# Kernel tuning notes

Hardware: AMD Instinct MI355X
Metric: run time of the kernel (lower is better)

The kernel has to match this reference:

```python
import jax, jax.numpy as jnp
import numpy as np

KH = KW = 3
PAD = 1
STRIDE = 1
C_IN = 32
C_OUT = 16
H = W = 64
B = 64
H_OUT = (H - KH + 2 * PAD) // STRIDE + 1
W_OUT = (W - KW + 2 * PAD) // STRIDE + 1
S = H_OUT * W_OUT
K = C_IN * KH * KW


def unfold_2d(x):
    # x: [B, C, H, W] -> [B, C*KH*KW, S], torch.nn.functional.unfold ordering
    xp = jnp.pad(x, ((0, 0), (0, 0), (PAD, PAD), (PAD, PAD)))
    patches = []
    for i in range(KH):
        for j in range(KW):
            patches.append(xp[:, :, i:i + H_OUT * STRIDE:STRIDE, j:j + W_OUT * STRIDE:STRIDE])
    u = jnp.stack(patches, axis=2)  # [B, C, KH*KW, H_OUT, W_OUT]
    return u.reshape(x.shape[0], K, S)


def setup_inputs() -> dict:
    key = jax.random.key(0)
    k1, k2, k3 = jax.random.split(key, 3)
    X = jax.random.normal(k1, (B, C_IN, H, W), dtype=jnp.float32)
    # kaiming normal (linear): std = 1/sqrt(fan_in), fan_in = K for each location's GEMM
    weight = jax.random.normal(k2, (S, K, C_OUT), dtype=jnp.float32) / jnp.sqrt(jnp.float32(K))
    # xavier uniform over [H_OUT, W_OUT]
    lim = np.sqrt(6.0 / (H_OUT + W_OUT))
    bias = jax.random.uniform(k3, (H_OUT, W_OUT), dtype=jnp.float32, minval=-lim, maxval=lim)
    return {"X": X, "weight": weight, "bias": bias}


def reference(X, weight, bias):
    ufld = unfold_2d(X)                               # [B, K, S]
    ufld = ufld + bias.reshape(1, 1, -1)              # bias added per-location to patches
    h = jnp.einsum('bks,skc->bcs', ufld, weight)      # per-location unshared GEMM
    return h.reshape(X.shape[0], C_OUT, H_OUT, W_OUT)
```

## Files before the change

### kernel.cpp

```cpp
#include <hip/hip_runtime.h>
#include <stdint.h>
#include <stddef.h>

#define HOUT 64
#define WOUT 64
#define CIN  32
#define COUT 16
#define BATCH 64
#define SLOC 4096
#define KTOT 288
#define HPAD 66

typedef __attribute__((ext_vector_type(8))) short  short8;
typedef __attribute__((ext_vector_type(4))) float  floatx4;

static __device__ __forceinline__ unsigned short f2bf(float f) {
    union { float f; unsigned int u; } v; v.f = f;
    unsigned int u = v.u;
    unsigned int r = (u + 0x7FFFu + ((u >> 16) & 1u)) >> 16;
    return (unsigned short)r;
}

__global__ __launch_bounds__(256) void zero_border_kernel(unsigned short* __restrict__ xt) {
    int bid = blockIdx.x;
    int h1, w1;
    if (bid < 66)       { h1 = 0;  w1 = bid; }
    else if (bid < 132) { h1 = 65; w1 = bid - 66; }
    else { int r = bid - 132; h1 = (r >> 1) + 1; w1 = (r & 1) ? 65 : 0; }
    uint4* dst = (uint4*)(xt + (size_t)(h1 * HPAD + w1) * 2048);
    dst[threadIdx.x] = uint4{0u, 0u, 0u, 0u};
}

__global__ __launch_bounds__(256) void transpose_kernel(const float* __restrict__ X,
                                                        unsigned short* __restrict__ xt) {
    int h = blockIdx.x;
    int b = blockIdx.y;
    int t = threadIdx.x;
    int w  = t >> 2;
    int cg = t & 3;

    const float* xb = X + (((size_t)b * CIN + cg * 8) * HOUT + h) * WOUT + w;
    unsigned short v[8];
#pragma unroll
    for (int j = 0; j < 8; ++j)
        v[j] = f2bf(xb[(size_t)j * HOUT * WOUT]);

    uint4 pack;
    pack.x = (unsigned)v[0] | ((unsigned)v[1] << 16);
    pack.y = (unsigned)v[2] | ((unsigned)v[3] << 16);
    pack.z = (unsigned)v[4] | ((unsigned)v[5] << 16);
    pack.w = (unsigned)v[6] | ((unsigned)v[7] << 16);

    *(uint4*)(xt + (size_t)((h + 1) * HPAD + (w + 1)) * 2048 + b * CIN + cg * 8) = pack;
}

__global__ __launch_bounds__(256, 4) void varconv_kernel(const unsigned short* __restrict__ xt,
                                                         const float* __restrict__ Wg,
                                                         const float* __restrict__ bias,
                                                         float* __restrict__ out) {
    __shared__ float lds[16 * 16 * 16];

    int id = blockIdx.x;
    int lo = id & 7;
    int q4 = (id >> 3) & 3;
    int g  = ((id >> 5) << 3) | lo;
    int s0 = g * 16;
    int y  = s0 >> 6;
    int x0 = s0 & 63;
    int B0 = q4 * 16;

    int lane = threadIdx.x & 63, wv = threadIdx.x >> 6;
    int q = lane >> 4;
    int n = lane & 15;

#pragma unroll
    for (int i = 0; i < 4; ++i) {
        int sl = wv * 4 + i;
        int s  = s0 + sl;
        int x  = x0 + sl;

        const float* wb = Wg + (size_t)s * (KTOT * COUT) + (size_t)(8 * q) * 9 * COUT + n;
        float w[9][8];
#pragma unroll
        for (int t = 0; t < 9; ++t)
#pragma unroll
            for (int j = 0; j < 8; ++j)
                w[t][j] = wb[(size_t)(j * 9 + t) * COUT];

        float csum = 0.f;
        short8 bf[9];
#pragma unroll
        for (int t = 0; t < 9; ++t)
#pragma unroll
            for (int j = 0; j < 8; ++j) {
                csum += w[t][j];
                bf[t][j] = (short)f2bf(w[t][j]);
            }
        csum += __shfl_xor(csum, 16, 64);
        csum += __shfl_xor(csum, 32, 64);
        float badd = bias[s] * csum;

        const unsigned short* ab = xt + (size_t)(B0 + n) * CIN + q * 8;
        floatx4 acc = {0.f, 0.f, 0.f, 0.f};
#pragma unroll
        for (int t = 0; t < 9; ++t) {
            const int cy = t / 3, cx = t % 3;
            int pix = (y + cy) * HPAD + (x + cx);
            short8 af = *(const short8*)(ab + (size_t)pix * 2048);
            acc = __builtin_amdgcn_mfma_f32_16x16x32_bf16(af, bf[t], acc, 0, 0, 0);
        }
        int slot = q ^ (n & 3);
        floatx4 v = {acc[0] + badd, acc[1] + badd, acc[2] + badd, acc[3] + badd};
        *(floatx4*)&lds[n * 256 + sl * 16 + slot * 4] = v;
    }

    __syncthreads();

    int c   = lane >> 2;
    int slg = lane & 3;
#pragma unroll
    for (int i2 = 0; i2 < 4; ++i2) {
        int ib   = wv * 4 + i2;
        int slot = (ib >> 2) ^ (c & 3);
        float o0[4];
#pragma unroll
        for (int e = 0; e < 4; ++e)
            o0[e] = lds[c * 256 + (slg * 4 + e) * 16 + slot * 4 + (ib & 3)];
        floatx4 o = {o0[0], o0[1], o0[2], o0[3]};
        *(floatx4*)(out + ((size_t)((B0 + ib) * COUT + c)) * SLOC + s0 + slg * 4) = o;
    }
}

extern "C" void kernel_launch(void* const* d_in, const int* in_sizes, int n_in,
                              void* d_out, int out_size, void* d_ws, size_t ws_size,
                              hipStream_t stream) {
    const float* X    = (const float*)d_in[0];
    const float* Wg   = (const float*)d_in[1];
    const float* bias = (const float*)d_in[2];
    float* out = (float*)d_out;

    unsigned short* xt = (unsigned short*)d_ws;

    zero_border_kernel<<<260, 256, 0, stream>>>(xt);
    transpose_kernel<<<dim3(64, 64), 256, 0, stream>>>(X, xt);
    varconv_kernel<<<1024, 256, 0, stream>>>(xt, Wg, bias, out);
}
```

Baseline: 173.8 us.

## Precompute bf16 packed weights and bias sums in a separate prep kernel

Adds a kernel that converts the per-location fp32 weights into bf16 in MFMA operand order and precomputes the bias-times-weight-sum per location and output channel. The main conv kernel then loads coalesced 16-byte weight fragments instead of doing strided fp32 gathers and conversions. It also batches all nine activation loads ahead of the MFMA chain. The cost is an extra launch and about twice the weight memory traffic, since the packed weights are written and read again every call.

```diff
diff --git a/kernel.cpp b/kernel.cpp
--- a/kernel.cpp
+++ b/kernel.cpp
@@ -54,9 +54,49 @@
     *(uint4*)(xt + (size_t)((h + 1) * HPAD + (w + 1)) * 2048 + b * CIN + cg * 8) = pack;
 }
 
+__global__ __launch_bounds__(576) void wprep_kernel(const float* __restrict__ Wg,
+                                                    const float* __restrict__ bias,
+                                                    uint4* __restrict__ wt,
+                                                    float* __restrict__ bsum) {
+    __shared__ float red[9][16];
+    int s    = blockIdx.x;
+    int t    = threadIdx.x >> 6;
+    int lane = threadIdx.x & 63;
+    int q = lane >> 4, n = lane & 15;
+
+    const float* wb = Wg + (size_t)s * (KTOT * COUT) + (size_t)((8 * q) * 9 + t) * COUT + n;
+    float w[8];
+#pragma unroll
+    for (int j = 0; j < 8; ++j)
+        w[j] = wb[(size_t)j * 9 * COUT];
+
+    float csum = 0.f;
+    unsigned short h[8];
+#pragma unroll
+    for (int j = 0; j < 8; ++j) { csum += w[j]; h[j] = f2bf(w[j]); }
+
+    uint4 pack;
+    pack.x = (unsigned)h[0] | ((unsigned)h[1] << 16);
+    pack.y = (unsigned)h[2] | ((unsigned)h[3] << 16);
+    pack.z = (unsigned)h[4] | ((unsigned)h[5] << 16);
+    pack.w = (unsigned)h[6] | ((unsigned)h[7] << 16);
+    wt[(size_t)(s * 9 + t) * 64 + lane] = pack;
+
+    csum += __shfl_xor(csum, 16, 64);
+    csum += __shfl_xor(csum, 32, 64);
+    if (lane < 16) red[t][n] = csum;
+    __syncthreads();
+    if (threadIdx.x < 16) {
+        float tot = 0.f;
+#pragma unroll
+        for (int tt = 0; tt < 9; ++tt) tot += red[tt][threadIdx.x];
+        bsum[s * COUT + threadIdx.x] = bias[s] * tot;
+    }
+}
+
 __global__ __launch_bounds__(256, 4) void varconv_kernel(const unsigned short* __restrict__ xt,
-                                                         const float* __restrict__ Wg,
-                                                         const float* __restrict__ bias,
+                                                         const uint4* __restrict__ wt,
+                                                         const float* __restrict__ bsum,
                                                          float* __restrict__ out) {
     __shared__ float lds[16 * 16 * 16];
 
@@ -79,36 +119,27 @@
         int s  = s0 + sl;
         int x  = x0 + sl;
 
-        const float* wb = Wg + (size_t)s * (KTOT * COUT) + (size_t)(8 * q) * 9 * COUT + n;
-        float w[9][8];
-#pragma unroll
-        for (int t = 0; t < 9; ++t)
-#pragma unroll
-            for (int j = 0; j < 8; ++j)
-                w[t][j] = wb[(size_t)(j * 9 + t) * COUT];
-
-        float csum = 0.f;
+        const uint4* wf = wt + (size_t)s * 9 * 64 + lane;
         short8 bf[9];
 #pragma unroll
         for (int t = 0; t < 9; ++t)
-#pragma unroll
-            for (int j = 0; j < 8; ++j) {
-                csum += w[t][j];
-                bf[t][j] = (short)f2bf(w[t][j]);
-            }
-        csum += __shfl_xor(csum, 16, 64);
-        csum += __shfl_xor(csum, 32, 64);
-        float badd = bias[s] * csum;
+            bf[t] = *(const short8*)(wf + t * 64);
+
+        float badd = bsum[s * COUT + n];
 
         const unsigned short* ab = xt + (size_t)(B0 + n) * CIN + q * 8;
-        floatx4 acc = {0.f, 0.f, 0.f, 0.f};
+        short8 af[9];
 #pragma unroll
         for (int t = 0; t < 9; ++t) {
             const int cy = t / 3, cx = t % 3;
-            int pix = (y + cy) * HPAD + (x + cx);
-            short8 af = *(const short8*)(ab + (size_t)pix * 2048);
-            acc = __builtin_amdgcn_mfma_f32_16x16x32_bf16(af, bf[t], acc, 0, 0, 0);
+            af[t] = *(const short8*)(ab + (size_t)((y + cy) * HPAD + (x + cx)) * 2048);
         }
+
+        floatx4 acc = {0.f, 0.f, 0.f, 0.f};
+#pragma unroll
+        for (int t = 0; t < 9; ++t)
+            acc = __builtin_amdgcn_mfma_f32_16x16x32_bf16(af[t], bf[t], acc, 0, 0, 0);
+
         int slot = q ^ (n & 3);
         floatx4 v = {acc[0] + badd, acc[1] + badd, acc[2] + badd, acc[3] + badd};
         *(floatx4*)&lds[n * 256 + sl * 16 + slot * 4] = v;
@@ -140,8 +171,11 @@
     float* out = (float*)d_out;
 
     unsigned short* xt = (unsigned short*)d_ws;
+    uint4* wt   = (uint4*)((char*)d_ws + 17842176);
+    float* bsum = (float*)((char*)d_ws + 17842176 + 37748736);
 
     zero_border_kernel<<<260, 256, 0, stream>>>(xt);
     transpose_kernel<<<dim3(64, 64), 256, 0, stream>>>(X, xt);
-    varconv_kernel<<<1024, 256, 0, stream>>>(xt, Wg, bias, out);
+    wprep_kernel<<<SLOC, 576, 0, stream>>>(Wg, bias, wt, bsum);
+    varconv_kernel<<<1024, 256, 0, stream>>>(xt, wt, bsum, out);
 }
```

New measurement: 166.9 us. 1.04x faster.
